# Performance work log

Hardware: AMD Instinct MI355X
Metric: run time of the kernel (lower is better)

## Reference

```python
import jax, jax.numpy as jnp
import numpy as np

DIM = 768
H = 12
DH = DIM // H          # 64
ROPE_DIM = (DH // 6) * 6   # 60
HALF = (ROPE_DIM // 3) // 2  # 10 freqs per axis
THETA = 10000.0
EPS = 1e-6


def rmsnorm(x, w):
    xf = x.astype(jnp.float32)
    var = jnp.mean(xf * xf, axis=-1, keepdims=True)
    return (w * (xf * jax.lax.rsqrt(var + EPS))).astype(x.dtype)


def rope_angles(positions):
    # positions: [B, N, 3] -> angles [B, N, 3*HALF]
    freqs = 1.0 / (THETA ** (jnp.arange(HALF, dtype=jnp.float32) / HALF))  # [HALF]
    # [B,N,3,1] * [1,1,1,HALF] -> [B,N,3,HALF] -> concat over axis order x,y,z
    ang = positions[..., :, None] * freqs[None, None, None, :]
    return ang.reshape(*positions.shape[:2], 3 * HALF)  # [B,N,30]


def apply_rope(t, cos, sin):
    # t: [B,N,H,ROPE_DIM]; cos/sin: [B,N,1,ROPE_DIM//2]
    B, N, Hh, D = t.shape
    tf = t.astype(jnp.float32).reshape(B, N, Hh, D // 2, 2)
    te, to = tf[..., 0], tf[..., 1]
    oe = te * cos - to * sin
    oo = te * sin + to * cos
    return jnp.stack([oe, oo], axis=-1).reshape(B, N, Hh, D).astype(t.dtype)


def setup_inputs() -> dict:
    key = jax.random.key(0)
    ks = jax.random.split(key, 5)
    B, N = 2, 2048
    x = jax.random.normal(ks[0], (B, N, DIM), dtype=jnp.float32)
    positions = jax.random.uniform(ks[1], (B, N, 3), dtype=jnp.float32)
    qkv_w = jax.random.normal(ks[2], (3 * DIM, DIM), dtype=jnp.float32) * (DIM ** -0.5)
    proj_w = jax.random.normal(ks[3], (DIM, DIM), dtype=jnp.float32) * (DIM ** -0.5)
    proj_b = jnp.zeros((DIM,), dtype=jnp.float32)
    qn_w = jnp.ones((DH,), dtype=jnp.float32)
    kn_w = jnp.ones((DH,), dtype=jnp.float32)
    return {"x": x, "positions": positions, "qkv_w": qkv_w, "proj_w": proj_w,
            "proj_b": proj_b, "qn_w": qn_w, "kn_w": kn_w}


def reference(x, positions, qkv_w, proj_w, proj_b, qn_w, kn_w):
    B, N, C = x.shape
    scale = DH ** -0.5
    qkv = (x @ qkv_w.T).reshape(B, N, 3, H, DH)
    q, k, v = qkv[:, :, 0], qkv[:, :, 1], qkv[:, :, 2]  # [B,N,H,DH]
    q = rmsnorm(q, qn_w)
    k = rmsnorm(k, kn_w)
    # 3D RoPE on first ROPE_DIM channels
    ang = rope_angles(positions)                 # [B,N,30]
    cos = jnp.cos(ang)[:, :, None, :]            # [B,N,1,30]
    sin = jnp.sin(ang)[:, :, None, :]
    q = jnp.concatenate([apply_rope(q[..., :ROPE_DIM], cos, sin), q[..., ROPE_DIM:]], axis=-1)
    k = jnp.concatenate([apply_rope(k[..., :ROPE_DIM], cos, sin), k[..., ROPE_DIM:]], axis=-1)
    attn = jnp.einsum('bqhd,bkhd->bhqk', q, k) * scale  # [B,H,N,N]
    attn = jax.nn.softmax(attn, axis=-1)
    out = jnp.einsum('bhqk,bkhd->bqhd', attn, v).reshape(B, N, C)
    return out @ proj_w.T + proj_b
```

## Files before the change

kernel.cpp:

```cpp
#include <hip/hip_runtime.h>
#include <hip/hip_bf16.h>
#include <math.h>

#define DIM 768
#define NH 12
#define DH 64
#define SEQ 2048
#define BATCH 2
#define TOK (BATCH*SEQ)
#define QKVN (3*DIM)

typedef __attribute__((ext_vector_type(8))) short bf16x8;
typedef __attribute__((ext_vector_type(4))) float f32x4;
typedef __attribute__((ext_vector_type(2))) unsigned int u32x2;
typedef unsigned short u16;

#define VM0 asm volatile("s_waitcnt vmcnt(0)" ::: "memory")
#define VM2 asm volatile("s_waitcnt vmcnt(2)" ::: "memory")
#define VM4 asm volatile("s_waitcnt vmcnt(4)" ::: "memory")
#define VM8 asm volatile("s_waitcnt vmcnt(8)" ::: "memory")
#define LGKM0 asm volatile("s_waitcnt lgkmcnt(0)" ::: "memory")
#define BAR() __builtin_amdgcn_s_barrier()

__device__ inline u16 f2bf(float f) {
  union { float f; unsigned u; } v; v.f = f;
  unsigned u = v.u;
  u += 0x7fffu + ((u >> 16) & 1u);
  return (u16)(u >> 16);
}

__device__ inline int pkbf(float a, float b) {
  __hip_bfloat162 h = __float22bfloat162_rn(make_float2(a, b));
  int r; __builtin_memcpy(&r, &h, 4); return r;
}

__global__ void conv_all(const float* __restrict__ a, u16* __restrict__ ao, int na4,
                         const float* __restrict__ b, u16* __restrict__ bo, int nb4,
                         const float* __restrict__ c, u16* __restrict__ co, int nc4,
                         const float* __restrict__ pos, float2* __restrict__ tab) {
  int i4 = blockIdx.x * blockDim.x + threadIdx.x;
  const int nconv = na4 + nb4 + nc4;
  if (i4 < nconv) {
    const float* src; u16* dst; int off;
    if (i4 < na4)            { src = a; dst = ao; off = i4; }
    else if (i4 < na4 + nb4) { src = b; dst = bo; off = i4 - na4; }
    else                     { src = c; dst = co; off = i4 - na4 - nb4; }
    float4 v = ((const float4*)src)[off];
    ushort4 o;
    o.x = f2bf(v.x); o.y = f2bf(v.y); o.z = f2bf(v.z); o.w = f2bf(v.w);
    ((ushort4*)dst)[off] = o;
    return;
  }
  int e = i4 - nconv;
  if (e >= TOK * 32) return;
  int t = e >> 5, p = e & 31;
  float cs = 1.f, sn = 0.f;
  if (p < 30) {
    int axis = p / 10, fi = p % 10;
    float freq = exp2f(-(float)fi * 1.3287712379549449f);
    float ang = pos[t * 3 + axis] * freq;
    cs = cosf(ang); sn = sinf(ang);
  }
  tab[e] = make_float2(cs, sn);
}

#define GLL(g, s) __builtin_amdgcn_global_load_lds((const __attribute__((address_space(1))) void*)(g), (__attribute__((address_space(3))) void*)(s), 16, 0, 0)

__global__ __launch_bounds__(256, 6) void gemm64(
    const u16* __restrict__ A, const u16* __restrict__ W,
    float* __restrict__ C, const float* __restrict__ bias,
    int M, int Nn, int K)
{
  __shared__ u16 As[2][64 * 32];
  __shared__ u16 Bs[2][64 * 32];
  const int t = threadIdx.x;
  const int w = t >> 6, l = t & 63;
  const int lr = l & 15, lg = l >> 4;
  const int wr = w >> 1, wc = w & 1;
  const int m0 = blockIdx.x * 64;
  const int n0 = blockIdx.y * 64;
  f32x4 acc[2][2] = {};
  const int srow = t >> 2;
  const int scol = (t & 3) * 8;
  const u16* aSrc = A + (size_t)(m0 + srow) * K + scol;
  const u16* bSrc = W + (size_t)(n0 + srow) * K + scol;
  const int NT = K / 32;

  GLL(aSrc, &As[0][w * 512]);
  GLL(bSrc, &Bs[0][w * 512]);

  for (int kt = 0; kt < NT; ++kt) {
    const int cur = kt & 1;
    if (kt + 1 < NT) {
      GLL(aSrc + (kt + 1) * 32, &As[cur ^ 1][w * 512]);
      GLL(bSrc + (kt + 1) * 32, &Bs[cur ^ 1][w * 512]);
      VM2;
    } else {
      VM0;
    }
    BAR();
    bf16x8 af[2], bff[2];
#pragma unroll
    for (int mi = 0; mi < 2; ++mi)
      af[mi] = *(const bf16x8*)(&As[cur][0] + (wr * 32 + mi * 16 + lr) * 32 + lg * 8);
#pragma unroll
    for (int ni = 0; ni < 2; ++ni)
      bff[ni] = *(const bf16x8*)(&Bs[cur][0] + (wc * 32 + ni * 16 + lr) * 32 + lg * 8);
#pragma unroll
    for (int mi = 0; mi < 2; ++mi)
#pragma unroll
      for (int ni = 0; ni < 2; ++ni)
        acc[mi][ni] = __builtin_amdgcn_mfma_f32_16x16x32_bf16(af[mi], bff[ni], acc[mi][ni], 0, 0, 0);
    LGKM0;
    BAR();
  }

#pragma unroll
  for (int mi = 0; mi < 2; ++mi)
#pragma unroll
    for (int ni = 0; ni < 2; ++ni)
#pragma unroll
      for (int r = 0; r < 4; ++r) {
        int row = m0 + wr * 32 + mi * 16 + lg * 4 + r;
        int col = n0 + wc * 32 + ni * 16 + lr;
        C[(size_t)row * Nn + col] = acc[mi][ni][r] + bias[col];
      }
}

__global__ __launch_bounds__(512, 4) void gemm_qkv(
    const u16* __restrict__ A, const u16* __restrict__ W,
    const float* __restrict__ qn_w, const float* __restrict__ kn_w,
    const float2* __restrict__ tab,
    u16* __restrict__ Qb, u16* __restrict__ Kb, u16* __restrict__ Vtb)
{
  __shared__ u16 As[2][128 * 32];
  __shared__ u16 Bs[2][128 * 32];
  const int K = DIM;
  const int t = threadIdx.x;
  const int w = t >> 6, l = t & 63;
  const int lr = l & 15, lg = l >> 4;
  const int wr = w >> 1, wc = w & 1;
  const int m0 = blockIdx.x * 128;
  const int n0 = blockIdx.y * 128;
  f32x4 acc[2][4] = {};
  const int srow = t >> 2;
  const int scol = (t & 3) * 8;
  const u16* aSrc = A + (size_t)(m0 + srow) * K + scol;
  const u16* bSrc = W + (size_t)(n0 + srow) * K + scol;
  const int NT = K / 32;

  GLL(aSrc, &As[0][w * 512]);
  GLL(bSrc, &Bs[0][w * 512]);

  for (int kt = 0; kt < NT; ++kt) {
    const int cur = kt & 1;
    if (kt + 1 < NT) {
      GLL(aSrc + (kt + 1) * 32, &As[cur ^ 1][w * 512]);
      GLL(bSrc + (kt + 1) * 32, &Bs[cur ^ 1][w * 512]);
      VM2;
    } else {
      VM0;
    }
    BAR();
    bf16x8 af[2], bff[4];
#pragma unroll
    for (int mi = 0; mi < 2; ++mi)
      af[mi] = *(const bf16x8*)(&As[cur][0] + (wr * 32 + mi * 16 + lr) * 32 + lg * 8);
#pragma unroll
    for (int ni = 0; ni < 4; ++ni)
      bff[ni] = *(const bf16x8*)(&Bs[cur][0] + (wc * 64 + ni * 16 + lr) * 32 + lg * 8);
#pragma unroll
    for (int mi = 0; mi < 2; ++mi)
#pragma unroll
      for (int ni = 0; ni < 4; ++ni)
        acc[mi][ni] = __builtin_amdgcn_mfma_f32_16x16x32_bf16(af[mi], bff[ni], acc[mi][ni], 0, 0, 0);
    LGKM0;
    BAR();
  }

  const int chunk = (n0 >> 6) + wc;
  const int tt = chunk / 12;
  const int h  = chunk % 12;
  const int bB = m0 >> 11;
  const int bh = bB * NH + h;

  if (tt == 2) {
#pragma unroll
    for (int mi = 0; mi < 2; ++mi) {
      const int nbase = (m0 + wr * 32 + mi * 16 + lg * 4) & 2047;
#pragma unroll
      for (int ni = 0; ni < 4; ++ni) {
        const int d = ni * 16 + lr;
        ushort4 o;
        o.x = f2bf(acc[mi][ni][0]); o.y = f2bf(acc[mi][ni][1]);
        o.z = f2bf(acc[mi][ni][2]); o.w = f2bf(acc[mi][ni][3]);
        *(ushort4*)(Vtb + ((size_t)bh * DH + d) * SEQ + nbase) = o;
      }
    }
  } else {
    const float* wv = (tt == 0 ? qn_w : kn_w);
    const float qs = (tt == 0 ? 0.125f * 1.4426950408889634f : 1.f);
    float wgt[4];
#pragma unroll
    for (int ni = 0; ni < 4; ++ni) wgt[ni] = wv[ni * 16 + lr];
    u16* outp = (tt == 0 ? Qb : Kb) + (size_t)bh * SEQ * DH;
#pragma unroll
    for (int mi = 0; mi < 2; ++mi) {
#pragma unroll
      for (int r = 0; r < 4; ++r) {
        float ss = 0.f;
#pragma unroll
        for (int ni = 0; ni < 4; ++ni) ss += acc[mi][ni][r] * acc[mi][ni][r];
        ss += __shfl_xor(ss, 1, 64);
        ss += __shfl_xor(ss, 2, 64);
        ss += __shfl_xor(ss, 4, 64);
        ss += __shfl_xor(ss, 8, 64);
        const float rms = rsqrtf(ss * (1.f / 64.f) + 1e-6f);
        const int trow = m0 + wr * 32 + mi * 16 + lg * 4 + r;
        const float2* tl = tab + trow * 32;
        u16* rowp = outp + (size_t)(trow & 2047) * DH;
#pragma unroll
        for (int ni = 0; ni < 4; ++ni) {
          const int d = ni * 16 + lr;
          float v = acc[mi][ni][r] * rms * wgt[ni];
          float vp = __shfl_xor(v, 1, 64);
          float2 cssn = tl[ni * 8 + (lr >> 1)];
          float sgn = (d & 1) ? cssn.y : -cssn.y;
          rowp[d] = f2bf((v * cssn.x + vp * sgn) * qs);
        }
      }
    }
  }
}

__global__ __launch_bounds__(256, 3) void attn(
    const u16* __restrict__ Qb, const u16* __restrict__ Kb,
    const u16* __restrict__ Vtb, u16* __restrict__ Ob)
{
  __shared__ u16 Ks[2][2][64 * 64];
  __shared__ u16 Vs[2][64 * 64];
  const int tid = threadIdx.x;
  const int w = tid >> 6, l = tid & 63;
  const int lr = l & 15, lg = l >> 4;
  const int qg = w & 1, half = w >> 1;
  const int wg = blockIdx.x;
  const int swz = (wg & 7) * 96 + (wg >> 3);
  const int bh = swz >> 5;
  const int q0 = (swz & 31) * 64;
  const u16* Qp = Qb + (size_t)bh * SEQ * DH;
  const u16* Kp = Kb + (size_t)bh * SEQ * DH;
  const u16* Vp = Vtb + (size_t)bh * DH * SEQ;

  const int qrA = q0 + qg * 32 + lr;
  const bf16x8 bq0a = *(const bf16x8*)(Qp + (size_t)qrA * DH + 8 * lg);
  const bf16x8 bq1a = *(const bf16x8*)(Qp + (size_t)qrA * DH + 32 + 8 * lg);
  const bf16x8 bq0b = *(const bf16x8*)(Qp + (size_t)(qrA + 16) * DH + 8 * lg);
  const bf16x8 bq1b = *(const bf16x8*)(Qp + (size_t)(qrA + 16) * DH + 32 + 8 * lg);

  const int srow = tid >> 3;
  const int sc16 = (tid & 7) ^ (srow & 7);
  const u16* kSrc = Kp + (size_t)srow * DH + sc16 * 8;
  const u16* vSrc = Vp + (size_t)srow * SEQ + sc16 * 8;

  const int frow = (lr & 3) | ((lr & 4) << 1) | ((lr & 8) >> 1);
  const int ksw = frow & 7;
  const int vsw = lr & 7;

  bf16x8 vone;
#pragma unroll
  for (int j = 0; j < 8; ++j) vone[j] = (short)0x3F80;

  f32x4 oaccA[4] = {}, oaccB[4] = {};
  f32x4 laccA = {}, laccB = {};

  GLL(kSrc,          &Ks[0][0][w * 512]);
  GLL(kSrc + 2048,   &Ks[0][0][w * 512 + 2048]);
  GLL(kSrc + 4096,   &Ks[0][1][w * 512]);
  GLL(kSrc + 6144,   &Ks[0][1][w * 512 + 2048]);
  GLL(vSrc,          &Vs[0][w * 512]);
  GLL(vSrc + 65536,  &Vs[0][w * 512 + 2048]);
  GLL(vSrc + 64,     &Vs[1][w * 512]);
  GLL(vSrc + 64 + 65536, &Vs[1][w * 512 + 2048]);

  for (int i = 0; i < 16; ++i) {
    const int p = i & 1;
    if (i + 1 < 16) {
      const size_t ko = (size_t)(2 * i + 2) * 4096;
      GLL(kSrc + ko,        &Ks[p ^ 1][0][w * 512]);
      GLL(kSrc + ko + 2048, &Ks[p ^ 1][0][w * 512 + 2048]);
      GLL(kSrc + ko + 4096, &Ks[p ^ 1][1][w * 512]);
      GLL(kSrc + ko + 6144, &Ks[p ^ 1][1][w * 512 + 2048]);
      VM8;
    } else {
      VM4;
    }
    BAR();
    const u16* Kt = &Ks[p][half][0];
    const u16* Vt = &Vs[half][0];

    f32x4 paccA[4] = {}, paccB[4] = {};
    __builtin_amdgcn_s_setprio(1);
#pragma unroll
    for (int c = 0; c < 4; ++c) {
      const int rbase = (16 * c + frow) * 64;
      bf16x8 ka = *(const bf16x8*)(Kt + rbase + ((lg ^ ksw) * 8));
      bf16x8 kb = *(const bf16x8*)(Kt + rbase + (((4 + lg) ^ ksw) * 8));
      paccA[c] = __builtin_amdgcn_mfma_f32_16x16x32_bf16(ka, bq0a, paccA[c], 0, 0, 0);
      paccA[c] = __builtin_amdgcn_mfma_f32_16x16x32_bf16(kb, bq1a, paccA[c], 0, 0, 0);
      paccB[c] = __builtin_amdgcn_mfma_f32_16x16x32_bf16(ka, bq0b, paccB[c], 0, 0, 0);
      paccB[c] = __builtin_amdgcn_mfma_f32_16x16x32_bf16(kb, bq1b, paccB[c], 0, 0, 0);
    }
    __builtin_amdgcn_s_setprio(0);

    if (i + 1 < 16) { VM4; } else { VM0; }
    LGKM0;
    BAR();

#pragma unroll
    for (int g = 0; g < 2; ++g) {
      const int clo = 2 * g, chi = 2 * g + 1;
      float pA[8], pB[8];
#pragma unroll
      for (int r = 0; r < 4; ++r) {
        pA[r]     = __builtin_amdgcn_exp2f(paccA[clo][r] - 12.f);
        pA[4 + r] = __builtin_amdgcn_exp2f(paccA[chi][r] - 12.f);
        pB[r]     = __builtin_amdgcn_exp2f(paccB[clo][r] - 12.f);
        pB[4 + r] = __builtin_amdgcn_exp2f(paccB[chi][r] - 12.f);
      }
      u32x2 a0 = __builtin_amdgcn_permlane32_swap((unsigned)pkbf(pA[0], pA[1]),
                                                  (unsigned)pkbf(pA[4], pA[5]), false, false);
      u32x2 a1 = __builtin_amdgcn_permlane32_swap((unsigned)pkbf(pA[2], pA[3]),
                                                  (unsigned)pkbf(pA[6], pA[7]), false, false);
      u32x2 b0 = __builtin_amdgcn_permlane32_swap((unsigned)pkbf(pB[0], pB[1]),
                                                  (unsigned)pkbf(pB[4], pB[5]), false, false);
      u32x2 b1 = __builtin_amdgcn_permlane32_swap((unsigned)pkbf(pB[2], pB[3]),
                                                  (unsigned)pkbf(pB[6], pB[7]), false, false);
      union { unsigned d[4]; bf16x8 v; } puA, puB;
      puA.d[0] = a0[0]; puA.d[1] = a1[0]; puA.d[2] = a0[1]; puA.d[3] = a1[1];
      puB.d[0] = b0[0]; puB.d[1] = b1[0]; puB.d[2] = b0[1]; puB.d[3] = b1[1];
      __builtin_amdgcn_s_setprio(1);
#pragma unroll
      for (int dt = 0; dt < 4; ++dt) {
        bf16x8 va = *(const bf16x8*)(Vt + (16 * dt + lr) * 64 + (((4 * g + lg) ^ vsw) * 8));
        oaccA[dt] = __builtin_amdgcn_mfma_f32_16x16x32_bf16(va, puA.v, oaccA[dt], 0, 0, 0);
        oaccB[dt] = __builtin_amdgcn_mfma_f32_16x16x32_bf16(va, puB.v, oaccB[dt], 0, 0, 0);
      }
      laccA = __builtin_amdgcn_mfma_f32_16x16x32_bf16(vone, puA.v, laccA, 0, 0, 0);
      laccB = __builtin_amdgcn_mfma_f32_16x16x32_bf16(vone, puB.v, laccB, 0, 0, 0);
      __builtin_amdgcn_s_setprio(0);
    }

    LGKM0;
    BAR();

    if (i + 1 < 16) {
      const size_t vo = (size_t)(2 * i + 2) * 64;
      GLL(vSrc + vo,              &Vs[0][w * 512]);
      GLL(vSrc + vo + 65536,      &Vs[0][w * 512 + 2048]);
      GLL(vSrc + vo + 64,         &Vs[1][w * 512]);
      GLL(vSrc + vo + 64 + 65536, &Vs[1][w * 512 + 2048]);
    }
  }

  float* scr = (float*)&Ks[0][0][0];
  const int sidA = (qg * 2 + 0) * 64 + l;
  const int sidB = (qg * 2 + 1) * 64 + l;
  if (half == 1) {
#pragma unroll
    for (int dt = 0; dt < 4; ++dt)
#pragma unroll
      for (int r = 0; r < 4; ++r) {
        scr[sidA * 17 + dt * 4 + r] = oaccA[dt][r];
        scr[sidB * 17 + dt * 4 + r] = oaccB[dt][r];
      }
    scr[sidA * 17 + 16] = laccA[0];
    scr[sidB * 17 + 16] = laccB[0];
  }
  __syncthreads();
  if (half == 1) return;
#pragma unroll
  for (int dt = 0; dt < 4; ++dt)
#pragma unroll
    for (int r = 0; r < 4; ++r) {
      oaccA[dt][r] += scr[sidA * 17 + dt * 4 + r];
      oaccB[dt][r] += scr[sidB * 17 + dt * 4 + r];
    }
  const float invA = 1.f / (laccA[0] + scr[sidA * 17 + 16]);
  const float invB = 1.f / (laccB[0] + scr[sidB * 17 + 16]);

  const int b = bh / NH, h = bh % NH;
  const int qA = q0 + qg * 32 + lr;
  size_t obA = (size_t)(b * SEQ + qA) * DIM + h * DH + 4 * lg;
  size_t obB = (size_t)(b * SEQ + qA + 16) * DIM + h * DH + 4 * lg;
#pragma unroll
  for (int dt = 0; dt < 4; ++dt) {
    ushort4 oA, oB;
    oA.x = f2bf(oaccA[dt][0] * invA); oA.y = f2bf(oaccA[dt][1] * invA);
    oA.z = f2bf(oaccA[dt][2] * invA); oA.w = f2bf(oaccA[dt][3] * invA);
    oB.x = f2bf(oaccB[dt][0] * invB); oB.y = f2bf(oaccB[dt][1] * invB);
    oB.z = f2bf(oaccB[dt][2] * invB); oB.w = f2bf(oaccB[dt][3] * invB);
    *(ushort4*)(Ob + obA + 16 * dt) = oA;
    *(ushort4*)(Ob + obB + 16 * dt) = oB;
  }
}

extern "C" void kernel_launch(void* const* d_in, const int* in_sizes, int n_in,
                              void* d_out, int out_size, void* d_ws, size_t ws_size,
                              hipStream_t stream) {
  const float* x      = (const float*)d_in[0];
  const float* pos    = (const float*)d_in[1];
  const float* qkv_w  = (const float*)d_in[2];
  const float* proj_w = (const float*)d_in[3];
  const float* proj_b = (const float*)d_in[4];
  const float* qn_w   = (const float*)d_in[5];
  const float* kn_w   = (const float*)d_in[6];
  char* ws = (char*)d_ws;
  u16*    xb    = (u16*)(ws + 0);
  u16*    wqkv  = (u16*)(ws + 6291456);
  u16*    wproj = (u16*)(ws + 9830400);
  float2* tab   = (float2*)(ws + 11010048);
  u16*    Qb    = (u16*)(ws + 12058624);
  u16*    Kb    = (u16*)(ws + 18350080);
  u16*    Vtb   = (u16*)(ws + 24641536);
  u16*    Ob    = (u16*)(ws + 30932992);
  float* out = (float*)d_out;

  const int na4 = TOK * DIM / 4, nb4 = QKVN * DIM / 4, nc4 = DIM * DIM / 4;
  const int ntot = na4 + nb4 + nc4 + TOK * 32;
  conv_all<<<(ntot + 255) / 256, 256, 0, stream>>>(
      x, xb, na4, qkv_w, wqkv, nb4, proj_w, wproj, nc4, pos, tab);

  dim3 g1(TOK / 128, QKVN / 128);
  gemm_qkv<<<g1, 512, 0, stream>>>(xb, wqkv, qn_w, kn_w, tab, Qb, Kb, Vtb);

  attn<<<SEQ / 64 * BATCH * NH, 256, 0, stream>>>(Qb, Kb, Vtb, Ob);

  dim3 g3(TOK / 64, DIM / 64);
  gemm64<<<g3, 256, 0, stream>>>(Ob, wproj, out, proj_b, TOK, DIM, DIM);
}
```

Measured before the change: 91.69 us.

## Deepen K-tile to 64 with swizzled LDS in GEMMs and prefetch K two tiles ahead

Both GEMM kernels now stage 64-wide K tiles with an XOR-swizzled LDS layout, which halves the number of barrier-separated iterations and is meant to avoid bank conflicts. Their launch-bound occupancy hints are lowered to match the larger LDS footprint. The attention kernel is rescheduled so K tiles are prefetched two iterations ahead, the barrier before the QK MFMA is removed, and the exp/pack work runs before waiting on V loads. The result is more memory latency hidden per barrier, at the cost of more LDS per block and lower occupancy.

```diff
diff --git a/kernel.cpp b/kernel.cpp
--- a/kernel.cpp
+++ b/kernel.cpp
@@ -16,9 +16,7 @@
 typedef unsigned short u16;
 
 #define VM0 asm volatile("s_waitcnt vmcnt(0)" ::: "memory")
-#define VM2 asm volatile("s_waitcnt vmcnt(2)" ::: "memory")
 #define VM4 asm volatile("s_waitcnt vmcnt(4)" ::: "memory")
-#define VM8 asm volatile("s_waitcnt vmcnt(8)" ::: "memory")
 #define LGKM0 asm volatile("s_waitcnt lgkmcnt(0)" ::: "memory")
 #define BAR() __builtin_amdgcn_s_barrier()
 
@@ -66,13 +64,13 @@
 
 #define GLL(g, s) __builtin_amdgcn_global_load_lds((const __attribute__((address_space(1))) void*)(g), (__attribute__((address_space(3))) void*)(s), 16, 0, 0)
 
-__global__ __launch_bounds__(256, 6) void gemm64(
+__global__ __launch_bounds__(256, 4) void gemm64(
     const u16* __restrict__ A, const u16* __restrict__ W,
     float* __restrict__ C, const float* __restrict__ bias,
     int M, int Nn, int K)
 {
-  __shared__ u16 As[2][64 * 32];
-  __shared__ u16 Bs[2][64 * 32];
+  __shared__ u16 As[2][64 * 64];
+  __shared__ u16 Bs[2][64 * 64];
   const int t = threadIdx.x;
   const int w = t >> 6, l = t & 63;
   const int lr = l & 15, lg = l >> 4;
@@ -80,37 +78,47 @@
   const int m0 = blockIdx.x * 64;
   const int n0 = blockIdx.y * 64;
   f32x4 acc[2][2] = {};
-  const int srow = t >> 2;
-  const int scol = (t & 3) * 8;
+  const int srow = t >> 3;
+  const int scol = (((t & 7) ^ (srow & 7)) * 8);
   const u16* aSrc = A + (size_t)(m0 + srow) * K + scol;
   const u16* bSrc = W + (size_t)(n0 + srow) * K + scol;
-  const int NT = K / 32;
-
-  GLL(aSrc, &As[0][w * 512]);
-  GLL(bSrc, &Bs[0][w * 512]);
+  const size_t r32 = (size_t)32 * K;
+  const int sw = lr & 7;
+  const int NT = K / 64;
+
+  GLL(aSrc,       &As[0][w * 512]);
+  GLL(aSrc + r32, &As[0][2048 + w * 512]);
+  GLL(bSrc,       &Bs[0][w * 512]);
+  GLL(bSrc + r32, &Bs[0][2048 + w * 512]);
 
   for (int kt = 0; kt < NT; ++kt) {
     const int cur = kt & 1;
     if (kt + 1 < NT) {
-      GLL(aSrc + (kt + 1) * 32, &As[cur ^ 1][w * 512]);
-      GLL(bSrc + (kt + 1) * 32, &Bs[cur ^ 1][w * 512]);
-      VM2;
+      const int k0 = (kt + 1) * 64;
+      GLL(aSrc + k0,       &As[cur ^ 1][w * 512]);
+      GLL(aSrc + r32 + k0, &As[cur ^ 1][2048 + w * 512]);
+      GLL(bSrc + k0,       &Bs[cur ^ 1][w * 512]);
+      GLL(bSrc + r32 + k0, &Bs[cur ^ 1][2048 + w * 512]);
+      VM4;
     } else {
       VM0;
     }
     BAR();
-    bf16x8 af[2], bff[2];
-#pragma unroll
-    for (int mi = 0; mi < 2; ++mi)
-      af[mi] = *(const bf16x8*)(&As[cur][0] + (wr * 32 + mi * 16 + lr) * 32 + lg * 8);
-#pragma unroll
-    for (int ni = 0; ni < 2; ++ni)
-      bff[ni] = *(const bf16x8*)(&Bs[cur][0] + (wc * 32 + ni * 16 + lr) * 32 + lg * 8);
-#pragma unroll
-    for (int mi = 0; mi < 2; ++mi)
+#pragma unroll
+    for (int kk = 0; kk < 2; ++kk) {
+      bf16x8 af[2], bff[2];
+#pragma unroll
+      for (int mi = 0; mi < 2; ++mi)
+        af[mi] = *(const bf16x8*)(&As[cur][0] + (wr * 32 + mi * 16 + lr) * 64 + (((kk * 4 + lg) ^ sw) * 8));
 #pragma unroll
       for (int ni = 0; ni < 2; ++ni)
-        acc[mi][ni] = __builtin_amdgcn_mfma_f32_16x16x32_bf16(af[mi], bff[ni], acc[mi][ni], 0, 0, 0);
+        bff[ni] = *(const bf16x8*)(&Bs[cur][0] + (wc * 32 + ni * 16 + lr) * 64 + (((kk * 4 + lg) ^ sw) * 8));
+#pragma unroll
+      for (int mi = 0; mi < 2; ++mi)
+#pragma unroll
+        for (int ni = 0; ni < 2; ++ni)
+          acc[mi][ni] = __builtin_amdgcn_mfma_f32_16x16x32_bf16(af[mi], bff[ni], acc[mi][ni], 0, 0, 0);
+    }
     LGKM0;
     BAR();
   }
@@ -127,14 +135,14 @@
       }
 }
 
-__global__ __launch_bounds__(512, 4) void gemm_qkv(
+__global__ __launch_bounds__(512, 2) void gemm_qkv(
     const u16* __restrict__ A, const u16* __restrict__ W,
     const float* __restrict__ qn_w, const float* __restrict__ kn_w,
     const float2* __restrict__ tab,
     u16* __restrict__ Qb, u16* __restrict__ Kb, u16* __restrict__ Vtb)
 {
-  __shared__ u16 As[2][128 * 32];
-  __shared__ u16 Bs[2][128 * 32];
+  __shared__ u16 As[2][128 * 64];
+  __shared__ u16 Bs[2][128 * 64];
   const int K = DIM;
   const int t = threadIdx.x;
   const int w = t >> 6, l = t & 63;
@@ -143,37 +151,47 @@
   const int m0 = blockIdx.x * 128;
   const int n0 = blockIdx.y * 128;
   f32x4 acc[2][4] = {};
-  const int srow = t >> 2;
-  const int scol = (t & 3) * 8;
+  const int srow = t >> 3;
+  const int scol = (((t & 7) ^ (srow & 7)) * 8);
   const u16* aSrc = A + (size_t)(m0 + srow) * K + scol;
   const u16* bSrc = W + (size_t)(n0 + srow) * K + scol;
-  const int NT = K / 32;
-
-  GLL(aSrc, &As[0][w * 512]);
-  GLL(bSrc, &Bs[0][w * 512]);
+  const size_t r64 = (size_t)64 * K;
+  const int sw = lr & 7;
+  const int NT = K / 64;
+
+  GLL(aSrc,       &As[0][w * 512]);
+  GLL(aSrc + r64, &As[0][4096 + w * 512]);
+  GLL(bSrc,       &Bs[0][w * 512]);
+  GLL(bSrc + r64, &Bs[0][4096 + w * 512]);
 
   for (int kt = 0; kt < NT; ++kt) {
     const int cur = kt & 1;
     if (kt + 1 < NT) {
-      GLL(aSrc + (kt + 1) * 32, &As[cur ^ 1][w * 512]);
-      GLL(bSrc + (kt + 1) * 32, &Bs[cur ^ 1][w * 512]);
-      VM2;
+      const int k0 = (kt + 1) * 64;
+      GLL(aSrc + k0,       &As[cur ^ 1][w * 512]);
+      GLL(aSrc + r64 + k0, &As[cur ^ 1][4096 + w * 512]);
+      GLL(bSrc + k0,       &Bs[cur ^ 1][w * 512]);
+      GLL(bSrc + r64 + k0, &Bs[cur ^ 1][4096 + w * 512]);
+      VM4;
     } else {
       VM0;
     }
     BAR();
-    bf16x8 af[2], bff[4];
-#pragma unroll
-    for (int mi = 0; mi < 2; ++mi)
-      af[mi] = *(const bf16x8*)(&As[cur][0] + (wr * 32 + mi * 16 + lr) * 32 + lg * 8);
-#pragma unroll
-    for (int ni = 0; ni < 4; ++ni)
-      bff[ni] = *(const bf16x8*)(&Bs[cur][0] + (wc * 64 + ni * 16 + lr) * 32 + lg * 8);
-#pragma unroll
-    for (int mi = 0; mi < 2; ++mi)
+#pragma unroll
+    for (int kk = 0; kk < 2; ++kk) {
+      bf16x8 af[2], bff[4];
+#pragma unroll
+      for (int mi = 0; mi < 2; ++mi)
+        af[mi] = *(const bf16x8*)(&As[cur][0] + (wr * 32 + mi * 16 + lr) * 64 + (((kk * 4 + lg) ^ sw) * 8));
 #pragma unroll
       for (int ni = 0; ni < 4; ++ni)
-        acc[mi][ni] = __builtin_amdgcn_mfma_f32_16x16x32_bf16(af[mi], bff[ni], acc[mi][ni], 0, 0, 0);
+        bff[ni] = *(const bf16x8*)(&Bs[cur][0] + (wc * 64 + ni * 16 + lr) * 64 + (((kk * 4 + lg) ^ sw) * 8));
+#pragma unroll
+      for (int mi = 0; mi < 2; ++mi)
+#pragma unroll
+        for (int ni = 0; ni < 4; ++ni)
+          acc[mi][ni] = __builtin_amdgcn_mfma_f32_16x16x32_bf16(af[mi], bff[ni], acc[mi][ni], 0, 0, 0);
+    }
     LGKM0;
     BAR();
   }
@@ -277,24 +295,19 @@
   GLL(kSrc + 2048,   &Ks[0][0][w * 512 + 2048]);
   GLL(kSrc + 4096,   &Ks[0][1][w * 512]);
   GLL(kSrc + 6144,   &Ks[0][1][w * 512 + 2048]);
-  GLL(vSrc,          &Vs[0][w * 512]);
-  GLL(vSrc + 65536,  &Vs[0][w * 512 + 2048]);
-  GLL(vSrc + 64,     &Vs[1][w * 512]);
+  VM0;
+  BAR();
+  GLL(vSrc,              &Vs[0][w * 512]);
+  GLL(vSrc + 65536,      &Vs[0][w * 512 + 2048]);
+  GLL(vSrc + 64,         &Vs[1][w * 512]);
   GLL(vSrc + 64 + 65536, &Vs[1][w * 512 + 2048]);
+  GLL(kSrc + 8192,   &Ks[1][0][w * 512]);
+  GLL(kSrc + 10240,  &Ks[1][0][w * 512 + 2048]);
+  GLL(kSrc + 12288,  &Ks[1][1][w * 512]);
+  GLL(kSrc + 14336,  &Ks[1][1][w * 512 + 2048]);
 
   for (int i = 0; i < 16; ++i) {
     const int p = i & 1;
-    if (i + 1 < 16) {
-      const size_t ko = (size_t)(2 * i + 2) * 4096;
-      GLL(kSrc + ko,        &Ks[p ^ 1][0][w * 512]);
-      GLL(kSrc + ko + 2048, &Ks[p ^ 1][0][w * 512 + 2048]);
-      GLL(kSrc + ko + 4096, &Ks[p ^ 1][1][w * 512]);
-      GLL(kSrc + ko + 6144, &Ks[p ^ 1][1][w * 512 + 2048]);
-      VM8;
-    } else {
-      VM4;
-    }
-    BAR();
     const u16* Kt = &Ks[p][half][0];
     const u16* Vt = &Vs[half][0];
 
@@ -312,43 +325,46 @@
     }
     __builtin_amdgcn_s_setprio(0);
 
-    if (i + 1 < 16) { VM4; } else { VM0; }
-    LGKM0;
-    BAR();
-
+    union { unsigned d[4]; bf16x8 v; } puA[2], puB[2];
 #pragma unroll
     for (int g = 0; g < 2; ++g) {
       const int clo = 2 * g, chi = 2 * g + 1;
-      float pA[8], pB[8];
+      float eA[8], eB[8];
 #pragma unroll
       for (int r = 0; r < 4; ++r) {
-        pA[r]     = __builtin_amdgcn_exp2f(paccA[clo][r] - 12.f);
-        pA[4 + r] = __builtin_amdgcn_exp2f(paccA[chi][r] - 12.f);
-        pB[r]     = __builtin_amdgcn_exp2f(paccB[clo][r] - 12.f);
-        pB[4 + r] = __builtin_amdgcn_exp2f(paccB[chi][r] - 12.f);
-      }
-      u32x2 a0 = __builtin_amdgcn_permlane32_swap((unsigned)pkbf(pA[0], pA[1]),
-                                                  (unsigned)pkbf(pA[4], pA[5]), false, false);
-      u32x2 a1 = __builtin_amdgcn_permlane32_swap((unsigned)pkbf(pA[2], pA[3]),
-                                                  (unsigned)pkbf(pA[6], pA[7]), false, false);
-      u32x2 b0 = __builtin_amdgcn_permlane32_swap((unsigned)pkbf(pB[0], pB[1]),
-                                                  (unsigned)pkbf(pB[4], pB[5]), false, false);
-      u32x2 b1 = __builtin_amdgcn_permlane32_swap((unsigned)pkbf(pB[2], pB[3]),
-                                                  (unsigned)pkbf(pB[6], pB[7]), false, false);
-      union { unsigned d[4]; bf16x8 v; } puA, puB;
-      puA.d[0] = a0[0]; puA.d[1] = a1[0]; puA.d[2] = a0[1]; puA.d[3] = a1[1];
-      puB.d[0] = b0[0]; puB.d[1] = b1[0]; puB.d[2] = b0[1]; puB.d[3] = b1[1];
-      __builtin_amdgcn_s_setprio(1);
+        eA[r]     = __builtin_amdgcn_exp2f(paccA[clo][r] - 12.f);
+        eA[4 + r] = __builtin_amdgcn_exp2f(paccA[chi][r] - 12.f);
+        eB[r]     = __builtin_amdgcn_exp2f(paccB[clo][r] - 12.f);
+        eB[4 + r] = __builtin_amdgcn_exp2f(paccB[chi][r] - 12.f);
+      }
+      u32x2 a0 = __builtin_amdgcn_permlane32_swap((unsigned)pkbf(eA[0], eA[1]),
+                                                  (unsigned)pkbf(eA[4], eA[5]), false, false);
+      u32x2 a1 = __builtin_amdgcn_permlane32_swap((unsigned)pkbf(eA[2], eA[3]),
+                                                  (unsigned)pkbf(eA[6], eA[7]), false, false);
+      u32x2 b0 = __builtin_amdgcn_permlane32_swap((unsigned)pkbf(eB[0], eB[1]),
+                                                  (unsigned)pkbf(eB[4], eB[5]), false, false);
+      u32x2 b1 = __builtin_amdgcn_permlane32_swap((unsigned)pkbf(eB[2], eB[3]),
+                                                  (unsigned)pkbf(eB[6], eB[7]), false, false);
+      puA[g].d[0] = a0[0]; puA[g].d[1] = a1[0]; puA[g].d[2] = a0[1]; puA[g].d[3] = a1[1];
+      puB[g].d[0] = b0[0]; puB[g].d[1] = b1[0]; puB[g].d[2] = b0[1]; puB[g].d[3] = b1[1];
+    }
+
+    VM0;
+    BAR();
+
+    __builtin_amdgcn_s_setprio(1);
+#pragma unroll
+    for (int g = 0; g < 2; ++g) {
 #pragma unroll
       for (int dt = 0; dt < 4; ++dt) {
         bf16x8 va = *(const bf16x8*)(Vt + (16 * dt + lr) * 64 + (((4 * g + lg) ^ vsw) * 8));
-        oaccA[dt] = __builtin_amdgcn_mfma_f32_16x16x32_bf16(va, puA.v, oaccA[dt], 0, 0, 0);
-        oaccB[dt] = __builtin_amdgcn_mfma_f32_16x16x32_bf16(va, puB.v, oaccB[dt], 0, 0, 0);
-      }
-      laccA = __builtin_amdgcn_mfma_f32_16x16x32_bf16(vone, puA.v, laccA, 0, 0, 0);
-      laccB = __builtin_amdgcn_mfma_f32_16x16x32_bf16(vone, puB.v, laccB, 0, 0, 0);
-      __builtin_amdgcn_s_setprio(0);
-    }
+        oaccA[dt] = __builtin_amdgcn_mfma_f32_16x16x32_bf16(va, puA[g].v, oaccA[dt], 0, 0, 0);
+        oaccB[dt] = __builtin_amdgcn_mfma_f32_16x16x32_bf16(va, puB[g].v, oaccB[dt], 0, 0, 0);
+      }
+      laccA = __builtin_amdgcn_mfma_f32_16x16x32_bf16(vone, puA[g].v, laccA, 0, 0, 0);
+      laccB = __builtin_amdgcn_mfma_f32_16x16x32_bf16(vone, puB[g].v, laccB, 0, 0, 0);
+    }
+    __builtin_amdgcn_s_setprio(0);
 
     LGKM0;
     BAR();
@@ -359,6 +375,13 @@
       GLL(vSrc + vo + 65536,      &Vs[0][w * 512 + 2048]);
       GLL(vSrc + vo + 64,         &Vs[1][w * 512]);
       GLL(vSrc + vo + 64 + 65536, &Vs[1][w * 512 + 2048]);
+    }
+    if (i + 2 < 16) {
+      const size_t ko = (size_t)(2 * i + 4) * 4096;
+      GLL(kSrc + ko,        &Ks[p][0][w * 512]);
+      GLL(kSrc + ko + 2048, &Ks[p][0][w * 512 + 2048]);
+      GLL(kSrc + ko + 4096, &Ks[p][1][w * 512]);
+      GLL(kSrc + ko + 6144, &Ks[p][1][w * 512 + 2048]);
     }
   }
 
```

After: 89.89 us. 2.0% less time.
